# Optimization experiments

Measured on AMD Instinct MI355X. Metric: run time of the kernel, lower is better.

## Reference

```python
import jax, jax.numpy as jnp
import numpy as np

W_MATCH, W_POS, W_COV = 1.0, 1.0, 0.1  # SetLoss init kwargs (w_rot unused in 3dpos path)


def setup_inputs() -> dict:
    key = jax.random.key(0)
    ks = jax.random.split(key, 6)
    bs, n, m = 4096, 31, 31
    B = bs * (n + 1)          # bs*(n+1) groups
    N = B * n                 # flattened rows
    # scores are 'in log space negative' -> use -softplus(randn)
    scores = -jax.nn.softplus(jax.random.normal(ks[0], (B, n + 1, m + 1), jnp.float32))
    indices = jax.random.randint(ks[1], (B, n, 1), -1, m)           # -1 = no prediction
    cov = jax.random.uniform(ks[2], (B, n, 1), jnp.float32, 0.1, 1.1)  # positive variances
    pos = jax.random.normal(ks[3], (B, n, 3), jnp.float32)
    pose = jax.random.normal(ks[4], (N, 7), jnp.float32)
    match = jax.random.randint(ks[5], (N, 1), -1, m)                # -1 = no label
    return {"scores": scores, "cov": cov, "pos": pos, "pose": pose,
            "indices": indices, "match": match}


def _masked_mean(vals, msk, default):
    cnt = msk.sum()
    s = jnp.where(msk, vals, 0.0).sum()
    return jnp.where(cnt > 0, s / jnp.maximum(cnt, 1).astype(vals.dtype), default)


def reference(scores, cov, pos, pose, indices, match):
    # SetLoss.forward(out, target, 'match_3dpos')
    m = scores.shape[2] - 1
    # ---- loss_match_func ----
    label_valid = match[:, 0] != -1                       # [N]
    li = jnp.where(match == -1, m, match)                 # route -1 to dustbin column m
    sc = scores[:, :-1, :].reshape(-1, m + 1)             # [N, m+1]
    cost = -jnp.take_along_axis(sc, li, axis=1)           # [N, 1]
    loss_match = cost.mean()
    oi = indices.reshape(-1, 1)
    success = (oi == match)[:, 0].astype(jnp.float32)     # [N]
    pred_valid = oi[:, 0] != -1
    recall = _masked_mean(success, label_valid, jnp.float32(1.0))
    precision = _masked_mean(success, pred_valid, jnp.float32(1.0))
    # ---- position MSE ----
    pos_f = pos.reshape(-1, 3)                            # [N, 3]
    d = pos_f - pose[:, :3]
    loss_pos = jnp.mean(d * d) * 3.0
    loss_rot = jnp.float32(0.0)
    # ---- diagonal-covariance NLL (loss_cov_func, dim=3, cov col repeated x3) ----
    # diag cov [c,c,c]: inverse = 1/c per entry, det = c**3
    c = cov.reshape(-1)                                   # [N]
    weighted = jnp.sum(d * d, axis=-1) / c                # diff^T Sigma^{-1} diff
    per = weighted + 3.0 * jnp.log(c) * 0.04              # + 0.04 * log det
    loss_cov = _masked_mean(per, pred_valid, jnp.float32(5.0))
    total = W_MATCH * loss_match + W_POS * loss_pos + W_COV * loss_cov
    return total, loss_match, loss_pos, loss_rot, loss_cov, precision, recall
```

## Files before the change

### kernel.cpp

```cpp
#include <hip/hip_runtime.h>
#include <hip/hip_bf16.h>

#define NRED 7

typedef int   int4v   __attribute__((ext_vector_type(4)));
typedef float float4v __attribute__((ext_vector_type(4)));

__device__ __forceinline__ float waveReduce(float v) {
#pragma unroll
    for (int o = 32; o > 0; o >>= 1) v += __shfl_down(v, o, 64);
    return v;
}

__device__ __forceinline__ void rowAcc(int r, int mt, int oi, float c,
                                       float px, float py, float pz,
                                       float qx, float qy, float qz,
                                       const float* __restrict__ scores,
                                       float acc[NRED]) {
    const unsigned ur = (unsigned)r;
    const unsigned b  = ur / 31u;
    const unsigned i  = ur - b * 31u;
    const int li = (mt < 0) ? 31 : mt;
    const float sc = __builtin_nontemporal_load(
        scores + (size_t)b * 1024u + i * 32u + (unsigned)li);
    acc[0] -= sc;

    const float succ = (oi == mt) ? 1.0f : 0.0f;
    const bool lv = (mt != -1);
    const bool pv = (oi != -1);
    acc[1] += lv ? 1.0f : 0.0f;
    acc[2] += lv ? succ : 0.0f;
    acc[3] += pv ? 1.0f : 0.0f;
    acc[4] += pv ? succ : 0.0f;

    const float dx = px - qx, dy = py - qy, dz = pz - qz;
    const float d2 = dx * dx + dy * dy + dz * dz;
    acc[5] += d2;
    if (pv) acc[6] += d2 / c + 0.12f * logf(c);
}

__global__ __launch_bounds__(256) void setloss_partial(
        const float* __restrict__ scores,
        const float* __restrict__ cov,
        const float* __restrict__ pos,
        const float* __restrict__ pose,
        const int* __restrict__ indices,
        const int* __restrict__ match,
        float* __restrict__ part,
        int N, int grid, int nChunk) {
    float acc[NRED];
#pragma unroll
    for (int k = 0; k < NRED; ++k) acc[k] = 0.0f;

    const int tstride = grid * 256;
    for (int chunk = blockIdx.x * 256 + threadIdx.x; chunk < nChunk; chunk += tstride) {
        const int base = chunk * 4;
        if (base + 3 < N) {
            const int4   mm = *(const int4*)  (match   + base);
            const int4   oo = *(const int4*)  (indices + base);
            const float4 cc = *(const float4*)(cov     + base);
            const float* pp = pos  + 3 * (size_t)base;
            const float4 p0 = *(const float4*)(pp + 0);
            const float4 p1 = *(const float4*)(pp + 4);
            const float4 p2 = *(const float4*)(pp + 8);
            const float* qq = pose + 7 * (size_t)base;
            const float4 q0 = *(const float4*)(qq + 0);
            const float4 q1 = *(const float4*)(qq + 4);
            const float4 q2 = *(const float4*)(qq + 8);
            const float4 q3 = *(const float4*)(qq + 12);
            const float4 q4 = *(const float4*)(qq + 16);
            const float4 q5 = *(const float4*)(qq + 20);

            rowAcc(base + 0, mm.x, oo.x, cc.x, p0.x, p0.y, p0.z, q0.x, q0.y, q0.z, scores, acc);
            rowAcc(base + 1, mm.y, oo.y, cc.y, p0.w, p1.x, p1.y, q1.w, q2.x, q2.y, scores, acc);
            rowAcc(base + 2, mm.z, oo.z, cc.z, p1.z, p1.w, p2.x, q3.z, q3.w, q4.x, scores, acc);
            rowAcc(base + 3, mm.w, oo.w, cc.w, p2.y, p2.z, p2.w, q5.y, q5.z, q5.w, scores, acc);
        } else {
            for (int r = base; r < N; ++r) {
                rowAcc(r, match[r], indices[r], cov[r],
                       pos[3 * (size_t)r + 0], pos[3 * (size_t)r + 1], pos[3 * (size_t)r + 2],
                       pose[7 * (size_t)r + 0], pose[7 * (size_t)r + 1], pose[7 * (size_t)r + 2],
                       scores, acc);
            }
        }
    }

    __shared__ float sdata[NRED][4];
    const int lane = threadIdx.x & 63;
    const int wave = threadIdx.x >> 6;
#pragma unroll
    for (int k = 0; k < NRED; ++k) {
        float v = waveReduce(acc[k]);
        if (lane == 0) sdata[k][wave] = v;
    }
    __syncthreads();
    if (threadIdx.x == 0) {
#pragma unroll
        for (int k = 0; k < NRED; ++k)
            part[(size_t)k * grid + blockIdx.x] =
                sdata[k][0] + sdata[k][1] + sdata[k][2] + sdata[k][3];
    }
}

__global__ void setloss_final(const float* __restrict__ part, int grid,
                              float* __restrict__ out, int N) {
    float acc[NRED];
#pragma unroll
    for (int k = 0; k < NRED; ++k) acc[k] = 0.0f;
    for (int t = threadIdx.x; t < grid; t += blockDim.x) {
#pragma unroll
        for (int k = 0; k < NRED; ++k) acc[k] += part[(size_t)k * grid + t];
    }
    __shared__ float sdata[NRED][4];
    const int lane = threadIdx.x & 63;
    const int wave = threadIdx.x >> 6;
#pragma unroll
    for (int k = 0; k < NRED; ++k) {
        float v = waveReduce(acc[k]);
        if (lane == 0) sdata[k][wave] = v;
    }
    __syncthreads();
    if (threadIdx.x == 0) {
        float s[NRED];
#pragma unroll
        for (int k = 0; k < NRED; ++k)
            s[k] = sdata[k][0] + sdata[k][1] + sdata[k][2] + sdata[k][3];

        const float fN = (float)N;
        const float loss_match = s[0] / fN;
        const float loss_pos   = s[5] / fN;
        const float recall     = (s[1] > 0.0f) ? s[2] / s[1] : 1.0f;
        const float precision  = (s[3] > 0.0f) ? s[4] / s[3] : 1.0f;
        const float loss_cov   = (s[3] > 0.0f) ? s[6] / s[3] : 5.0f;

        out[0] = loss_match + loss_pos + 0.1f * loss_cov;
        out[1] = loss_match;
        out[2] = loss_pos;
        out[3] = 0.0f;
        out[4] = loss_cov;
        out[5] = precision;
        out[6] = recall;
    }
}

extern "C" void kernel_launch(void* const* d_in, const int* in_sizes, int n_in,
                              void* d_out, int out_size, void* d_ws, size_t ws_size,
                              hipStream_t stream) {
    const float* scores  = (const float*)d_in[0];
    const float* cov     = (const float*)d_in[1];
    const float* pos     = (const float*)d_in[2];
    const float* pose    = (const float*)d_in[3];
    const int*   indices = (const int*)d_in[4];
    const int*   match   = (const int*)d_in[5];
    float* out = (float*)d_out;

    const int N = in_sizes[5];
    const int nChunk = (N + 3) / 4;

    int grid = (nChunk + 255) / 256;
    const size_t cap = ws_size / ((size_t)NRED * sizeof(float));
    if ((size_t)grid > cap) grid = (int)cap;
    if (grid < 1) grid = 1;

    float* part = (float*)d_ws;

    setloss_partial<<<grid, 256, 0, stream>>>(scores, cov, pos, pose, indices,
                                              match, part, N, grid, nChunk);
    setloss_final<<<1, 256, 0, stream>>>(part, grid, out, N);
}
```

Measured before the change: 113.4 us.

## Use lane-strided row mapping and issue scores gathers before other loads

Rows are now assigned so that consecutive lanes handle consecutive rows, with four rows per thread strided by 64. Before, each thread took four contiguous rows loaded as float4 vectors. The match values are loaded first so the scattered scores gathers can be issued early and overlap the other loads. Each thread now makes scalar, coalesced loads instead of wide vector loads. The grid-stride loop is removed, so correctness depends on grid covering N/1024 blocks; if the workspace cap shrinks the grid, rows would be silently skipped.

```diff
diff --git a/kernel.cpp b/kernel.cpp
--- a/kernel.cpp
+++ b/kernel.cpp
@@ -3,40 +3,10 @@
 
 #define NRED 7
 
-typedef int   int4v   __attribute__((ext_vector_type(4)));
-typedef float float4v __attribute__((ext_vector_type(4)));
-
 __device__ __forceinline__ float waveReduce(float v) {
 #pragma unroll
     for (int o = 32; o > 0; o >>= 1) v += __shfl_down(v, o, 64);
     return v;
-}
-
-__device__ __forceinline__ void rowAcc(int r, int mt, int oi, float c,
-                                       float px, float py, float pz,
-                                       float qx, float qy, float qz,
-                                       const float* __restrict__ scores,
-                                       float acc[NRED]) {
-    const unsigned ur = (unsigned)r;
-    const unsigned b  = ur / 31u;
-    const unsigned i  = ur - b * 31u;
-    const int li = (mt < 0) ? 31 : mt;
-    const float sc = __builtin_nontemporal_load(
-        scores + (size_t)b * 1024u + i * 32u + (unsigned)li);
-    acc[0] -= sc;
-
-    const float succ = (oi == mt) ? 1.0f : 0.0f;
-    const bool lv = (mt != -1);
-    const bool pv = (oi != -1);
-    acc[1] += lv ? 1.0f : 0.0f;
-    acc[2] += lv ? succ : 0.0f;
-    acc[3] += pv ? 1.0f : 0.0f;
-    acc[4] += pv ? succ : 0.0f;
-
-    const float dx = px - qx, dy = py - qy, dz = pz - qz;
-    const float d2 = dx * dx + dy * dy + dz * dz;
-    acc[5] += d2;
-    if (pv) acc[6] += d2 / c + 0.12f * logf(c);
 }
 
 __global__ __launch_bounds__(256) void setloss_partial(
@@ -47,47 +17,76 @@
         const int* __restrict__ indices,
         const int* __restrict__ match,
         float* __restrict__ part,
-        int N, int grid, int nChunk) {
+        int N, int grid) {
     float acc[NRED];
 #pragma unroll
     for (int k = 0; k < NRED; ++k) acc[k] = 0.0f;
 
-    const int tstride = grid * 256;
-    for (int chunk = blockIdx.x * 256 + threadIdx.x; chunk < nChunk; chunk += tstride) {
-        const int base = chunk * 4;
-        if (base + 3 < N) {
-            const int4   mm = *(const int4*)  (match   + base);
-            const int4   oo = *(const int4*)  (indices + base);
-            const float4 cc = *(const float4*)(cov     + base);
-            const float* pp = pos  + 3 * (size_t)base;
-            const float4 p0 = *(const float4*)(pp + 0);
-            const float4 p1 = *(const float4*)(pp + 4);
-            const float4 p2 = *(const float4*)(pp + 8);
-            const float* qq = pose + 7 * (size_t)base;
-            const float4 q0 = *(const float4*)(qq + 0);
-            const float4 q1 = *(const float4*)(qq + 4);
-            const float4 q2 = *(const float4*)(qq + 8);
-            const float4 q3 = *(const float4*)(qq + 12);
-            const float4 q4 = *(const float4*)(qq + 16);
-            const float4 q5 = *(const float4*)(qq + 20);
+    const int lane = threadIdx.x & 63;
+    const int wave = threadIdx.x >> 6;
+    const int wbase = blockIdx.x * 1024 + wave * 256;
 
-            rowAcc(base + 0, mm.x, oo.x, cc.x, p0.x, p0.y, p0.z, q0.x, q0.y, q0.z, scores, acc);
-            rowAcc(base + 1, mm.y, oo.y, cc.y, p0.w, p1.x, p1.y, q1.w, q2.x, q2.y, scores, acc);
-            rowAcc(base + 2, mm.z, oo.z, cc.z, p1.z, p1.w, p2.x, q3.z, q3.w, q4.x, scores, acc);
-            rowAcc(base + 3, mm.w, oo.w, cc.w, p2.y, p2.z, p2.w, q5.y, q5.z, q5.w, scores, acc);
+    int  r[4];  bool vld[4];
+#pragma unroll
+    for (int k = 0; k < 4; ++k) { r[k] = wbase + 64 * k + lane; vld[k] = r[k] < N; }
+
+    int mt[4];
+#pragma unroll
+    for (int k = 0; k < 4; ++k) mt[k] = vld[k] ? match[r[k]] : -1;
+
+    float sc[4];
+#pragma unroll
+    for (int k = 0; k < 4; ++k) {
+        if (vld[k]) {
+            const unsigned ur = (unsigned)r[k];
+            const unsigned b  = ur / 31u;
+            const unsigned i  = ur - b * 31u;
+            const int li = (mt[k] < 0) ? 31 : mt[k];
+            sc[k] = __builtin_nontemporal_load(
+                scores + (size_t)b * 1024u + i * 32u + (unsigned)li);
+        } else sc[k] = 0.0f;
+    }
+
+    int oi[4]; float cc[4];
+#pragma unroll
+    for (int k = 0; k < 4; ++k) oi[k] = vld[k] ? indices[r[k]] : -1;
+#pragma unroll
+    for (int k = 0; k < 4; ++k) cc[k] = vld[k] ? cov[r[k]] : 1.0f;
+
+    float P[4][3], Q[4][3];
+#pragma unroll
+    for (int k = 0; k < 4; ++k) {
+        const size_t rp = 3 * (size_t)r[k];
+        const size_t rq = 7 * (size_t)r[k];
+        if (vld[k]) {
+            P[k][0] = pos[rp + 0];  P[k][1] = pos[rp + 1];  P[k][2] = pos[rp + 2];
+            Q[k][0] = pose[rq + 0]; Q[k][1] = pose[rq + 1]; Q[k][2] = pose[rq + 2];
         } else {
-            for (int r = base; r < N; ++r) {
-                rowAcc(r, match[r], indices[r], cov[r],
-                       pos[3 * (size_t)r + 0], pos[3 * (size_t)r + 1], pos[3 * (size_t)r + 2],
-                       pose[7 * (size_t)r + 0], pose[7 * (size_t)r + 1], pose[7 * (size_t)r + 2],
-                       scores, acc);
-            }
+            P[k][0] = P[k][1] = P[k][2] = 0.0f;
+            Q[k][0] = Q[k][1] = Q[k][2] = 0.0f;
         }
     }
 
+#pragma unroll
+    for (int k = 0; k < 4; ++k) {
+        if (!vld[k]) continue;
+        acc[0] -= sc[k];
+        const float succ = (oi[k] == mt[k]) ? 1.0f : 0.0f;
+        const bool lv = (mt[k] != -1);
+        const bool pv = (oi[k] != -1);
+        acc[1] += lv ? 1.0f : 0.0f;
+        acc[2] += lv ? succ : 0.0f;
+        acc[3] += pv ? 1.0f : 0.0f;
+        acc[4] += pv ? succ : 0.0f;
+        const float dx = P[k][0] - Q[k][0];
+        const float dy = P[k][1] - Q[k][1];
+        const float dz = P[k][2] - Q[k][2];
+        const float d2 = dx * dx + dy * dy + dz * dz;
+        acc[5] += d2;
+        if (pv) acc[6] += d2 / cc[k] + 0.12f * logf(cc[k]);
+    }
+
     __shared__ float sdata[NRED][4];
-    const int lane = threadIdx.x & 63;
-    const int wave = threadIdx.x >> 6;
 #pragma unroll
     for (int k = 0; k < NRED; ++k) {
         float v = waveReduce(acc[k]);
@@ -155,9 +154,8 @@
     float* out = (float*)d_out;
 
     const int N = in_sizes[5];
-    const int nChunk = (N + 3) / 4;
 
-    int grid = (nChunk + 255) / 256;
+    int grid = (N + 1023) / 1024;
     const size_t cap = ws_size / ((size_t)NRED * sizeof(float));
     if ((size_t)grid > cap) grid = (int)cap;
     if (grid < 1) grid = 1;
@@ -165,6 +163,6 @@
     float* part = (float*)d_ws;
 
     setloss_partial<<<grid, 256, 0, stream>>>(scores, cov, pos, pose, indices,
-                                              match, part, N, grid, nChunk);
+                                              match, part, N, grid);
     setloss_final<<<1, 256, 0, stream>>>(part, grid, out, N);
 }
```

Measured after the change: 120.1 us. +6.0%, slower.
